# Optimization experiments

Hardware: AMD Instinct MI355X
Metric: run time of the kernel (lower is better)

Reference implementation:

```python
import jax, jax.numpy as jnp
import numpy as np

MARGIN = 0.5


def setup_inputs() -> dict:
    key = jax.random.key(0)
    k1, k2, k3, k4, k5 = jax.random.split(key, 5)
    N, V, D = 4096, 10000, 128
    return {
        "context_batch": jax.random.normal(k1, (N, V), dtype=jnp.float32),
        "response_batch": jax.random.normal(k2, (N, V), dtype=jnp.float32),
        "neg_response_batch": jax.random.normal(k3, (N, V), dtype=jnp.float32),
        # uniform(-1, 1) init as in reset_parameters
        "context_embedding": jax.random.uniform(k4, (D, V), minval=-1.0, maxval=1.0, dtype=jnp.float32),
        "response_embedding": jax.random.uniform(k5, (D, V), minval=-1.0, maxval=1.0, dtype=jnp.float32),
    }


def reference(context_batch, response_batch, neg_response_batch,
              context_embedding, response_embedding):
    # cont_rep: [N, D] = (E_c @ X^T)^T
    cont_rep = context_batch @ context_embedding.T          # [N, D]
    resp_rep = response_batch @ response_embedding.T        # [N, D]
    neg_resp_rep = neg_response_batch @ response_embedding.T  # [N, D]
    # diag(cont_rep @ resp_rep^T) == row-wise dot product (same math, O(N*D))
    f_pos = jnp.sum(cont_rep * resp_rep, axis=-1)           # [N]
    f_neg = jnp.sum(cont_rep * neg_resp_rep, axis=-1)       # [N]
    loss = jnp.sum(jax.nn.relu(f_neg - f_pos + MARGIN))
    return f_pos, f_neg, loss
```

## Files before the change

kernel.cpp:

```cpp
#include <hip/hip_runtime.h>
#include <hip/hip_bf16.h>
#include <cstdint>

#define VDIM 10000
#define VPAD 10016
#define NROW 4096
#define DDIM 128
#define KSTEPS 313
#define KSPLIT 8
#define KCHUNK 40

typedef __attribute__((ext_vector_type(8))) short bf16x8;
typedef __attribute__((ext_vector_type(4))) float f32x4;

__device__ __forceinline__ unsigned short f2bf(float f) {
    union { float f; unsigned u; } v; v.f = f;
    unsigned u = v.u;
    unsigned r = (u + 0x7FFFu + ((u >> 16) & 1u)) >> 16;
    return (unsigned short)r;
}

__global__ __launch_bounds__(256) void convert_emb(
    const float* __restrict__ ec, const float* __restrict__ er,
    unsigned short* __restrict__ out)
{
    int idx8 = (blockIdx.x * 256 + threadIdx.x) * 8;
    const int total = 2 * DDIM * VPAD;
    if (idx8 >= total) return;
    int e   = idx8 / (DDIM * VPAD);
    int rem = idx8 - e * (DDIM * VPAD);
    int row = rem / VPAD;
    int k   = rem - row * VPAD;
    unsigned short o[8];
    if (k < VDIM) {
        const float* src = (e ? er : ec) + row * VDIM + k;
        #pragma unroll
        for (int j = 0; j < 8; ++j) o[j] = f2bf(src[j]);
    } else {
        #pragma unroll
        for (int j = 0; j < 8; ++j) o[j] = 0;
    }
    *reinterpret_cast<bf16x8*>(out + idx8) = *reinterpret_cast<const bf16x8*>(o);
}

__global__ __launch_bounds__(256, 3) void gemm_rep(
    const float* __restrict__ a0, const float* __restrict__ a1,
    const float* __restrict__ a2,
    const unsigned short* __restrict__ emb,
    float* __restrict__ reps)
{
    __shared__ short bLds[2][DDIM][40];

    const int rb = blockIdx.x;
    const int s  = blockIdx.y;
    const int kc = blockIdx.z;
    const float* A = (s == 0) ? a0 : (s == 1 ? a1 : a2);
    const unsigned short* E = emb + (size_t)(s == 0 ? 0 : 1) * (DDIM * VPAD);

    const int tid  = threadIdx.x;
    const int wave = tid >> 6;
    const int lane = tid & 63;
    const int l15  = lane & 15;
    const int quad = lane >> 4;

    const int scol  = tid >> 1;
    const int shalf = tid & 1;
    const unsigned short* sp = E + (size_t)scol * VPAD + shalf * 16;

    const int kt0 = kc * KCHUNK;
    const int kt1 = (kt0 + KCHUNK < KSTEPS) ? (kt0 + KCHUNK) : KSTEPS;

    const int r0 = rb * 128 + wave * 32;
    const float* ap0 = A + (size_t)(r0 + l15) * VDIM;
    const float* ap1 = A + (size_t)(r0 + 16 + l15) * VDIM;

    f32x4 acc[2][8];
    #pragma unroll
    for (int rf = 0; rf < 2; ++rf)
        #pragma unroll
        for (int ct = 0; ct < 8; ++ct) acc[rf][ct] = (f32x4){0.f, 0.f, 0.f, 0.f};

    bf16x8 sA0, sA1, sB0, sB1;
    f32x4 ar0, ar1, ar2, ar3;
    bf16x8 af0, af1;

#define CLAMPK(KT) (((KT) < KSTEPS - 1) ? (KT) : (KSTEPS - 1))

#define GLOADB(sa, sb, KT) do {                                        \
        const unsigned short* q_ = sp + (size_t)(KT) * 32;             \
        sa = *reinterpret_cast<const bf16x8*>(q_);                     \
        sb = *reinterpret_cast<const bf16x8*>(q_ + 8);                 \
    } while (0)

#define GLOADA(KT) do {                                                \
        int koA_ = (KT) * 32 + quad * 8;                               \
        int koC_ = koA_ > (VDIM - 8) ? (VDIM - 8) : koA_;              \
        ar0 = *reinterpret_cast<const f32x4*>(ap0 + koC_);             \
        ar1 = *reinterpret_cast<const f32x4*>(ap0 + koC_ + 4);         \
        ar2 = *reinterpret_cast<const f32x4*>(ap1 + koC_);             \
        ar3 = *reinterpret_cast<const f32x4*>(ap1 + koC_ + 4);         \
    } while (0)

#define CONVA(KT) do {                                                 \
        int ko_ = (KT) * 32 + quad * 8;                                \
        if (ko_ < VDIM) {                                              \
            af0[0]=(short)f2bf(ar0[0]); af0[1]=(short)f2bf(ar0[1]);    \
            af0[2]=(short)f2bf(ar0[2]); af0[3]=(short)f2bf(ar0[3]);    \
            af0[4]=(short)f2bf(ar1[0]); af0[5]=(short)f2bf(ar1[1]);    \
            af0[6]=(short)f2bf(ar1[2]); af0[7]=(short)f2bf(ar1[3]);    \
            af1[0]=(short)f2bf(ar2[0]); af1[1]=(short)f2bf(ar2[1]);    \
            af1[2]=(short)f2bf(ar2[2]); af1[3]=(short)f2bf(ar2[3]);    \
            af1[4]=(short)f2bf(ar3[0]); af1[5]=(short)f2bf(ar3[1]);    \
            af1[6]=(short)f2bf(ar3[2]); af1[7]=(short)f2bf(ar3[3]);    \
        } else {                                                       \
            af0 = (bf16x8){0,0,0,0,0,0,0,0};                           \
            af1 = (bf16x8){0,0,0,0,0,0,0,0};                           \
        }                                                              \
    } while (0)

#define DSWRITE(BUF, sa, sb) do {                                      \
        *reinterpret_cast<bf16x8*>(&bLds[BUF][scol][shalf * 16])     = sa; \
        *reinterpret_cast<bf16x8*>(&bLds[BUF][scol][shalf * 16 + 8]) = sb; \
    } while (0)

#define BODY(T, P, Sa, Sb) do {                                        \
        CONVA(T);                       \
        GLOADA((T) + 1);                \
        DSWRITE((P) ^ 1, Sa, Sb);        \
        GLOADB(Sa, Sb, CLAMPK((T) + 3));   \
        bf16x8 b0_ = *reinterpret_cast<const bf16x8*>(&bLds[P][ 0 + l15][quad * 8]); \
        bf16x8 b1_ = *reinterpret_cast<const bf16x8*>(&bLds[P][16 + l15][quad * 8]); \
        bf16x8 b2_ = *reinterpret_cast<const bf16x8*>(&bLds[P][32 + l15][quad * 8]); \
        bf16x8 b3_ = *reinterpret_cast<const bf16x8*>(&bLds[P][48 + l15][quad * 8]); \
        acc[0][0] = __builtin_amdgcn_mfma_f32_16x16x32_bf16(af0, b0_, acc[0][0], 0, 0, 0); \
        acc[1][0] = __builtin_amdgcn_mfma_f32_16x16x32_bf16(af1, b0_, acc[1][0], 0, 0, 0); \
        acc[0][1] = __builtin_amdgcn_mfma_f32_16x16x32_bf16(af0, b1_, acc[0][1], 0, 0, 0); \
        acc[1][1] = __builtin_amdgcn_mfma_f32_16x16x32_bf16(af1, b1_, acc[1][1], 0, 0, 0); \
        acc[0][2] = __builtin_amdgcn_mfma_f32_16x16x32_bf16(af0, b2_, acc[0][2], 0, 0, 0); \
        acc[1][2] = __builtin_amdgcn_mfma_f32_16x16x32_bf16(af1, b2_, acc[1][2], 0, 0, 0); \
        acc[0][3] = __builtin_amdgcn_mfma_f32_16x16x32_bf16(af0, b3_, acc[0][3], 0, 0, 0); \
        acc[1][3] = __builtin_amdgcn_mfma_f32_16x16x32_bf16(af1, b3_, acc[1][3], 0, 0, 0); \
        bf16x8 b4_ = *reinterpret_cast<const bf16x8*>(&bLds[P][ 64 + l15][quad * 8]); \
        bf16x8 b5_ = *reinterpret_cast<const bf16x8*>(&bLds[P][ 80 + l15][quad * 8]); \
        bf16x8 b6_ = *reinterpret_cast<const bf16x8*>(&bLds[P][ 96 + l15][quad * 8]); \
        bf16x8 b7_ = *reinterpret_cast<const bf16x8*>(&bLds[P][112 + l15][quad * 8]); \
        acc[0][4] = __builtin_amdgcn_mfma_f32_16x16x32_bf16(af0, b4_, acc[0][4], 0, 0, 0); \
        acc[1][4] = __builtin_amdgcn_mfma_f32_16x16x32_bf16(af1, b4_, acc[1][4], 0, 0, 0); \
        acc[0][5] = __builtin_amdgcn_mfma_f32_16x16x32_bf16(af0, b5_, acc[0][5], 0, 0, 0); \
        acc[1][5] = __builtin_amdgcn_mfma_f32_16x16x32_bf16(af1, b5_, acc[1][5], 0, 0, 0); \
        acc[0][6] = __builtin_amdgcn_mfma_f32_16x16x32_bf16(af0, b6_, acc[0][6], 0, 0, 0); \
        acc[1][6] = __builtin_amdgcn_mfma_f32_16x16x32_bf16(af1, b6_, acc[1][6], 0, 0, 0); \
        acc[0][7] = __builtin_amdgcn_mfma_f32_16x16x32_bf16(af0, b7_, acc[0][7], 0, 0, 0); \
        acc[1][7] = __builtin_amdgcn_mfma_f32_16x16x32_bf16(af1, b7_, acc[1][7], 0, 0, 0); \
        asm volatile("s_barrier" ::: "memory");                        \
    } while (0)

    {
        bf16x8 p0_, p1_;
        GLOADB(p0_, p1_, kt0);
        DSWRITE(0, p0_, p1_);
        GLOADB(sA0, sA1, CLAMPK(kt0 + 1));
        GLOADB(sB0, sB1, CLAMPK(kt0 + 2));
        GLOADA(kt0);
        asm volatile("s_waitcnt lgkmcnt(0)" ::: "memory");
        asm volatile("s_barrier" ::: "memory");
    }

    int kt = kt0;
    while (true) {
        BODY(kt, 0, sA0, sA1);
        if (++kt >= kt1) break;
        BODY(kt, 1, sB0, sB1);
        if (++kt >= kt1) break;
    }

    float* rp = reps + (size_t)s * NROW * DDIM + (size_t)r0 * DDIM;
    #pragma unroll
    for (int rf = 0; rf < 2; ++rf)
        #pragma unroll
        for (int ct = 0; ct < 8; ++ct)
            #pragma unroll
            for (int r = 0; r < 4; ++r)
                atomicAdd(rp + (size_t)(rf * 16 + quad * 4 + r) * DDIM + ct * 16 + l15,
                          acc[rf][ct][r]);
#undef BODY
#undef DSWRITE
#undef CONVA
#undef GLOADA
#undef GLOADB
#undef CLAMPK
}

__global__ __launch_bounds__(256) void finalize(
    const float* __restrict__ reps, float* __restrict__ out)
{
    __shared__ float ls[4];
    const int wid  = threadIdx.x >> 6;
    const int lane = threadIdx.x & 63;
    const int row  = blockIdx.x * 4 + wid;

    const float* c = reps + (size_t)row * DDIM + 2 * lane;
    const float* r = c + (size_t)NROW * DDIM;
    const float* n = r + (size_t)NROW * DDIM;
    const float2 cv = *reinterpret_cast<const float2*>(c);
    const float2 rv = *reinterpret_cast<const float2*>(r);
    const float2 nv = *reinterpret_cast<const float2*>(n);

    float fp = cv.x * rv.x + cv.y * rv.y;
    float fn = cv.x * nv.x + cv.y * nv.y;
    #pragma unroll
    for (int off = 32; off > 0; off >>= 1) {
        fp += __shfl_down(fp, off);
        fn += __shfl_down(fn, off);
    }
    if (lane == 0) {
        out[row]        = fp;
        out[NROW + row] = fn;
        float t = fn - fp + 0.5f;
        ls[wid] = t > 0.f ? t : 0.f;
    }
    __syncthreads();
    if (threadIdx.x == 0)
        atomicAdd(out + 2 * NROW, ls[0] + ls[1] + ls[2] + ls[3]);
}

extern "C" void kernel_launch(void* const* d_in, const int* in_sizes, int n_in,
                              void* d_out, int out_size, void* d_ws, size_t ws_size,
                              hipStream_t stream)
{
    const float* cb  = (const float*)d_in[0];
    const float* rbb = (const float*)d_in[1];
    const float* nb  = (const float*)d_in[2];
    const float* ce  = (const float*)d_in[3];
    const float* re  = (const float*)d_in[4];
    float* out = (float*)d_out;

    unsigned short* emb = (unsigned short*)d_ws;
    const size_t embBytes = (size_t)2 * DDIM * VPAD * sizeof(unsigned short);
    float* reps = (float*)((char*)d_ws + embBytes);
    const size_t repBytes = (size_t)3 * NROW * DDIM * sizeof(float);

    convert_emb<<<dim3((2 * DDIM * VPAD / 8) / 256), dim3(256), 0, stream>>>(ce, re, emb);
    hipMemsetAsync(reps, 0, repBytes, stream);
    hipMemsetAsync(out + 2 * NROW, 0, sizeof(float), stream);
    gemm_rep<<<dim3(NROW / 128, 3, KSPLIT), dim3(256), 0, stream>>>(cb, rbb, nb, emb, reps);
    finalize<<<dim3(NROW / 4), dim3(256), 0, stream>>>(reps, out);
}
```

Before: 207.3 us.

## Halve GEMM row tile to 64 and raise occupancy with simpler prefetch pipeline

```diff
diff --git a/kernel.cpp b/kernel.cpp
--- a/kernel.cpp
+++ b/kernel.cpp
@@ -9,6 +9,7 @@
 #define KSTEPS 313
 #define KSPLIT 8
 #define KCHUNK 40
+#define RBLK 64
 
 typedef __attribute__((ext_vector_type(8))) short bf16x8;
 typedef __attribute__((ext_vector_type(4))) float f32x4;
@@ -43,7 +44,7 @@
     *reinterpret_cast<bf16x8*>(out + idx8) = *reinterpret_cast<const bf16x8*>(o);
 }
 
-__global__ __launch_bounds__(256, 3) void gemm_rep(
+__global__ __launch_bounds__(256, 6) void gemm_rep(
     const float* __restrict__ a0, const float* __restrict__ a1,
     const float* __restrict__ a2,
     const unsigned short* __restrict__ emb,
@@ -70,21 +71,16 @@
     const int kt0 = kc * KCHUNK;
     const int kt1 = (kt0 + KCHUNK < KSTEPS) ? (kt0 + KCHUNK) : KSTEPS;
 
-    const int r0 = rb * 128 + wave * 32;
-    const float* ap0 = A + (size_t)(r0 + l15) * VDIM;
-    const float* ap1 = A + (size_t)(r0 + 16 + l15) * VDIM;
-
-    f32x4 acc[2][8];
+    const int r0 = rb * RBLK + wave * 16;
+    const float* ap = A + (size_t)(r0 + l15) * VDIM;
+
+    f32x4 acc[8];
     #pragma unroll
-    for (int rf = 0; rf < 2; ++rf)
-        #pragma unroll
-        for (int ct = 0; ct < 8; ++ct) acc[rf][ct] = (f32x4){0.f, 0.f, 0.f, 0.f};
-
-    bf16x8 sA0, sA1, sB0, sB1;
-    f32x4 ar0, ar1, ar2, ar3;
-    bf16x8 af0, af1;
-
-#define CLAMPK(KT) (((KT) < KSTEPS - 1) ? (KT) : (KSTEPS - 1))
+    for (int ct = 0; ct < 8; ++ct) acc[ct] = (f32x4){0.f, 0.f, 0.f, 0.f};
+
+    bf16x8 sB0, sB1;
+    f32x4 ar0, ar1;
+    bf16x8 af;
 
 #define GLOADB(sa, sb, KT) do {                                        \
         const unsigned short* q_ = sp + (size_t)(KT) * 32;             \
@@ -95,26 +91,19 @@
 #define GLOADA(KT) do {                                                \
         int koA_ = (KT) * 32 + quad * 8;                               \
         int koC_ = koA_ > (VDIM - 8) ? (VDIM - 8) : koA_;              \
-        ar0 = *reinterpret_cast<const f32x4*>(ap0 + koC_);             \
-        ar1 = *reinterpret_cast<const f32x4*>(ap0 + koC_ + 4);         \
-        ar2 = *reinterpret_cast<const f32x4*>(ap1 + koC_);             \
-        ar3 = *reinterpret_cast<const f32x4*>(ap1 + koC_ + 4);         \
+        ar0 = *reinterpret_cast<const f32x4*>(ap + koC_);              \
+        ar1 = *reinterpret_cast<const f32x4*>(ap + koC_ + 4);          \
     } while (0)
 
 #define CONVA(KT) do {                                                 \
         int ko_ = (KT) * 32 + quad * 8;                                \
         if (ko_ < VDIM) {                                              \
-            af0[0]=(short)f2bf(ar0[0]); af0[1]=(short)f2bf(ar0[1]);    \
-            af0[2]=(short)f2bf(ar0[2]); af0[3]=(short)f2bf(ar0[3]);    \
-            af0[4]=(short)f2bf(ar1[0]); af0[5]=(short)f2bf(ar1[1]);    \
-            af0[6]=(short)f2bf(ar1[2]); af0[7]=(short)f2bf(ar1[3]);    \
-            af1[0]=(short)f2bf(ar2[0]); af1[1]=(short)f2bf(ar2[1]);    \
-            af1[2]=(short)f2bf(ar2[2]); af1[3]=(short)f2bf(ar2[3]);    \
-            af1[4]=(short)f2bf(ar3[0]); af1[5]=(short)f2bf(ar3[1]);    \
-            af1[6]=(short)f2bf(ar3[2]); af1[7]=(short)f2bf(ar3[3]);    \
+            af[0]=(short)f2bf(ar0[0]); af[1]=(short)f2bf(ar0[1]);      \
+            af[2]=(short)f2bf(ar0[2]); af[3]=(short)f2bf(ar0[3]);      \
+            af[4]=(short)f2bf(ar1[0]); af[5]=(short)f2bf(ar1[1]);      \
+            af[6]=(short)f2bf(ar1[2]); af[7]=(short)f2bf(ar1[3]);      \
         } else {                                                       \
-            af0 = (bf16x8){0,0,0,0,0,0,0,0};                           \
-            af1 = (bf16x8){0,0,0,0,0,0,0,0};                           \
+            af = (bf16x8){0,0,0,0,0,0,0,0};                            \
         }                                                              \
     } while (0)
 
@@ -123,72 +112,62 @@
         *reinterpret_cast<bf16x8*>(&bLds[BUF][scol][shalf * 16 + 8]) = sb; \
     } while (0)
 
-#define BODY(T, P, Sa, Sb) do {                                        \
-        CONVA(T);                       \
-        GLOADA((T) + 1);                \
-        DSWRITE((P) ^ 1, Sa, Sb);        \
-        GLOADB(Sa, Sb, CLAMPK((T) + 3));   \
+#define BODY(T, P) do {                                                \
+        CONVA(T);                         \
+        if ((T) + 1 < kt1) {                                           \
+            GLOADA((T) + 1);                       \
+            DSWRITE((P) ^ 1, sB0, sB1);             \
+        }                                                              \
+        if ((T) + 2 < kt1) GLOADB(sB0, sB1, (T) + 2);                  \
         bf16x8 b0_ = *reinterpret_cast<const bf16x8*>(&bLds[P][ 0 + l15][quad * 8]); \
         bf16x8 b1_ = *reinterpret_cast<const bf16x8*>(&bLds[P][16 + l15][quad * 8]); \
         bf16x8 b2_ = *reinterpret_cast<const bf16x8*>(&bLds[P][32 + l15][quad * 8]); \
         bf16x8 b3_ = *reinterpret_cast<const bf16x8*>(&bLds[P][48 + l15][quad * 8]); \
-        acc[0][0] = __builtin_amdgcn_mfma_f32_16x16x32_bf16(af0, b0_, acc[0][0], 0, 0, 0); \
-        acc[1][0] = __builtin_amdgcn_mfma_f32_16x16x32_bf16(af1, b0_, acc[1][0], 0, 0, 0); \
-        acc[0][1] = __builtin_amdgcn_mfma_f32_16x16x32_bf16(af0, b1_, acc[0][1], 0, 0, 0); \
-        acc[1][1] = __builtin_amdgcn_mfma_f32_16x16x32_bf16(af1, b1_, acc[1][1], 0, 0, 0); \
-        acc[0][2] = __builtin_amdgcn_mfma_f32_16x16x32_bf16(af0, b2_, acc[0][2], 0, 0, 0); \
-        acc[1][2] = __builtin_amdgcn_mfma_f32_16x16x32_bf16(af1, b2_, acc[1][2], 0, 0, 0); \
-        acc[0][3] = __builtin_amdgcn_mfma_f32_16x16x32_bf16(af0, b3_, acc[0][3], 0, 0, 0); \
-        acc[1][3] = __builtin_amdgcn_mfma_f32_16x16x32_bf16(af1, b3_, acc[1][3], 0, 0, 0); \
+        acc[0] = __builtin_amdgcn_mfma_f32_16x16x32_bf16(af, b0_, acc[0], 0, 0, 0); \
+        acc[1] = __builtin_amdgcn_mfma_f32_16x16x32_bf16(af, b1_, acc[1], 0, 0, 0); \
+        acc[2] = __builtin_amdgcn_mfma_f32_16x16x32_bf16(af, b2_, acc[2], 0, 0, 0); \
+        acc[3] = __builtin_amdgcn_mfma_f32_16x16x32_bf16(af, b3_, acc[3], 0, 0, 0); \
         bf16x8 b4_ = *reinterpret_cast<const bf16x8*>(&bLds[P][ 64 + l15][quad * 8]); \
         bf16x8 b5_ = *reinterpret_cast<const bf16x8*>(&bLds[P][ 80 + l15][quad * 8]); \
         bf16x8 b6_ = *reinterpret_cast<const bf16x8*>(&bLds[P][ 96 + l15][quad * 8]); \
         bf16x8 b7_ = *reinterpret_cast<const bf16x8*>(&bLds[P][112 + l15][quad * 8]); \
-        acc[0][4] = __builtin_amdgcn_mfma_f32_16x16x32_bf16(af0, b4_, acc[0][4], 0, 0, 0); \
-        acc[1][4] = __builtin_amdgcn_mfma_f32_16x16x32_bf16(af1, b4_, acc[1][4], 0, 0, 0); \
-        acc[0][5] = __builtin_amdgcn_mfma_f32_16x16x32_bf16(af0, b5_, acc[0][5], 0, 0, 0); \
-        acc[1][5] = __builtin_amdgcn_mfma_f32_16x16x32_bf16(af1, b5_, acc[1][5], 0, 0, 0); \
-        acc[0][6] = __builtin_amdgcn_mfma_f32_16x16x32_bf16(af0, b6_, acc[0][6], 0, 0, 0); \
-        acc[1][6] = __builtin_amdgcn_mfma_f32_16x16x32_bf16(af1, b6_, acc[1][6], 0, 0, 0); \
-        acc[0][7] = __builtin_amdgcn_mfma_f32_16x16x32_bf16(af0, b7_, acc[0][7], 0, 0, 0); \
-        acc[1][7] = __builtin_amdgcn_mfma_f32_16x16x32_bf16(af1, b7_, acc[1][7], 0, 0, 0); \
-        asm volatile("s_barrier" ::: "memory");                        \
+        acc[4] = __builtin_amdgcn_mfma_f32_16x16x32_bf16(af, b4_, acc[4], 0, 0, 0); \
+        acc[5] = __builtin_amdgcn_mfma_f32_16x16x32_bf16(af, b5_, acc[5], 0, 0, 0); \
+        acc[6] = __builtin_amdgcn_mfma_f32_16x16x32_bf16(af, b6_, acc[6], 0, 0, 0); \
+        acc[7] = __builtin_amdgcn_mfma_f32_16x16x32_bf16(af, b7_, acc[7], 0, 0, 0); \
     } while (0)
 
     {
         bf16x8 p0_, p1_;
         GLOADB(p0_, p1_, kt0);
         DSWRITE(0, p0_, p1_);
-        GLOADB(sA0, sA1, CLAMPK(kt0 + 1));
-        GLOADB(sB0, sB1, CLAMPK(kt0 + 2));
+        GLOADB(sB0, sB1, kt0 + 1);
         GLOADA(kt0);
-        asm volatile("s_waitcnt lgkmcnt(0)" ::: "memory");
-        asm volatile("s_barrier" ::: "memory");
+        __syncthreads();
     }
 
     int kt = kt0;
     while (true) {
-        BODY(kt, 0, sA0, sA1);
+        BODY(kt, 0);
         if (++kt >= kt1) break;
-        BODY(kt, 1, sB0, sB1);
+        __syncthreads();
+        BODY(kt, 1);
         if (++kt >= kt1) break;
+        __syncthreads();
     }
 
     float* rp = reps + (size_t)s * NROW * DDIM + (size_t)r0 * DDIM;
     #pragma unroll
-    for (int rf = 0; rf < 2; ++rf)
+    for (int ct = 0; ct < 8; ++ct)
         #pragma unroll
-        for (int ct = 0; ct < 8; ++ct)
-            #pragma unroll
-            for (int r = 0; r < 4; ++r)
-                atomicAdd(rp + (size_t)(rf * 16 + quad * 4 + r) * DDIM + ct * 16 + l15,
-                          acc[rf][ct][r]);
+        for (int r = 0; r < 4; ++r)
+            atomicAdd(rp + (size_t)(quad * 4 + r) * DDIM + ct * 16 + l15,
+                      acc[ct][r]);
 #undef BODY
 #undef DSWRITE
 #undef CONVA
 #undef GLOADA
 #undef GLOADB
-#undef CLAMPK
 }
 
 __global__ __launch_bounds__(256) void finalize(
@@ -243,6 +222,6 @@
     convert_emb<<<dim3((2 * DDIM * VPAD / 8) / 256), dim3(256), 0, stream>>>(ce, re, emb);
     hipMemsetAsync(reps, 0, repBytes, stream);
     hipMemsetAsync(out + 2 * NROW, 0, sizeof(float), stream);
-    gemm_rep<<<dim3(NROW / 128, 3, KSPLIT), dim3(256), 0, stream>>>(cb, rbb, nb, emb, reps);
+    gemm_rep<<<dim3(NROW / RBLK, 3, KSPLIT), dim3(256), 0, stream>>>(cb, rbb, nb, emb, reps);
     finalize<<<dim3(NROW / 4), dim3(256), 0, stream>>>(reps, out);
 }
```

New measurement: 202.1 us. 1.03x faster.
